# Kernel optimization log

Measured on AMD Instinct MI355X. Metric: run time of the kernel, lower is better.

The kernel has to match this reference:

```python
import jax, jax.numpy as jnp
import numpy as np

B, N, FIN, FOUT = 32, 1024, 128, 128
NEG_SLOPE = 0.01  # torch nn.LeakyReLU default


def setup_inputs() -> dict:
    key = jax.random.key(0)
    k1, k2, k3, k4 = jax.random.split(key, 4)
    node_mat = jax.random.normal(k1, (B, N, FIN), dtype=jnp.float32)
    adj_mat = jax.random.uniform(k2, (B, N, N), dtype=jnp.float32)
    # nn.Linear(FIN, FOUT): weight [FOUT, FIN], bias [FOUT]
    bound = 1.0 / np.sqrt(FIN)
    W = jax.random.uniform(k3, (FOUT, FIN), minval=-bound, maxval=bound, dtype=jnp.float32)
    b = jax.random.uniform(k4, (FOUT,), minval=-bound, maxval=bound, dtype=jnp.float32)
    return {"node_mat": node_mat, "adj_mat": adj_mat, "W": W, "b": b}


def reference(node_mat, adj_mat, W, b):
    # degree per node: row-sum of adjacency [B, N, 1]
    n_neighbors = adj_mat.sum(axis=-1, keepdims=True)
    # D^-1 A : the original builds eye*(1/deg) then bmm; algebraically a row scaling
    norm_adj = adj_mat / n_neighbors                      # [B, N, N]
    agg = jnp.einsum('bnm,bmf->bnf', norm_adj, node_mat)  # [B, N, FIN]
    out = jnp.einsum('bnf,of->bno', agg, W) + b           # [B, N, FOUT]
    return jnp.where(out >= 0, out, NEG_SLOPE * out)      # LeakyReLU
```

## Files before the change

### kernel.cpp

```cpp
#include <hip/hip_runtime.h>
#include <cstdint>
#include <cstddef>

#define BB   32
#define NN   1024
#define FIN  128
#define FOUT 128

typedef __attribute__((ext_vector_type(8))) short bf16x8;
typedef __attribute__((ext_vector_type(4))) float f32x4;

__device__ __forceinline__ unsigned int f2bf(float f) {
    union { float f; unsigned int u; } v; v.f = f;
    unsigned int u = v.u;
    return (u + 0x7FFFu + ((u >> 16) & 1u)) >> 16;
}
__device__ __forceinline__ unsigned int pack2(float a, float b) {
    return f2bf(a) | (f2bf(b) << 16);
}

__global__ __launch_bounds__(256) void y_kernel(const float* __restrict__ node,
                                                const float* __restrict__ W,
                                                unsigned short* __restrict__ Yt) {
    __shared__ unsigned short Wlds[128 * 136];
    __shared__ unsigned short Nlds[64 * 136];

    const int tid = threadIdx.x;
    const int bid = blockIdx.x;
    const int b   = bid >> 4;
    const int m0  = (bid & 15) * 64;

    #pragma unroll
    for (int i = 0; i < 16; ++i) {
        const int idx = i * 256 + tid;
        const int row = idx >> 5;
        const int c   = (idx & 31) * 4;
        float4 v = ((const float4*)W)[idx];
        uint2 p; p.x = pack2(v.x, v.y); p.y = pack2(v.z, v.w);
        *(uint2*)&Wlds[row * 136 + c] = p;
    }
    {
        const float* base = node + ((size_t)b * NN + m0) * FIN;
        #pragma unroll
        for (int i = 0; i < 8; ++i) {
            const int idx = i * 256 + tid;
            const int row = idx >> 5;
            const int c   = (idx & 31) * 4;
            float4 v = *(const float4*)(base + row * FIN + c);
            uint2 p; p.x = pack2(v.x, v.y); p.y = pack2(v.z, v.w);
            *(uint2*)&Nlds[row * 136 + c] = p;
        }
    }
    __syncthreads();

    const int w = tid >> 6, lane = tid & 63;
    const int wo = w * 32;
    const int lcol = lane & 15, lk = (lane >> 4) * 8;

    f32x4 acc[2][4] = {};
    #pragma unroll
    for (int kc = 0; kc < 4; ++kc) {
        const int kof = kc * 32 + lk;
        bf16x8 a[2], bb[4];
        #pragma unroll
        for (int mi = 0; mi < 2; ++mi)
            a[mi] = *(const bf16x8*)&Wlds[(wo + mi*16 + lcol) * 136 + kof];
        #pragma unroll
        for (int ni = 0; ni < 4; ++ni)
            bb[ni] = *(const bf16x8*)&Nlds[(ni*16 + lcol) * 136 + kof];
        #pragma unroll
        for (int mi = 0; mi < 2; ++mi)
            #pragma unroll
            for (int ni = 0; ni < 4; ++ni)
                acc[mi][ni] = __builtin_amdgcn_mfma_f32_16x16x32_bf16(
                    a[mi], bb[ni], acc[mi][ni], 0, 0, 0);
    }
    __syncthreads();

    unsigned short* Ylds = Wlds;
    const int rq = (lane >> 4) * 4;
    #pragma unroll
    for (int mi = 0; mi < 2; ++mi)
        #pragma unroll
        for (int ni = 0; ni < 4; ++ni)
            #pragma unroll
            for (int r = 0; r < 4; ++r) {
                const int o = wo + mi * 16 + rq + r;
                const int m = ni * 16 + lcol;
                Ylds[o * 72 + m] = (unsigned short)f2bf(acc[mi][ni][r]);
            }
    __syncthreads();

    {
        const int oq = tid >> 3, c = (tid & 7) * 8;
        #pragma unroll
        for (int j = 0; j < 4; ++j) {
            const int o = oq + 32 * j;
            uint4 v = *(const uint4*)&Ylds[o * 72 + c];
            *(uint4*)(Yt + ((size_t)b * FOUT + o) * NN + m0 + c) = v;
        }
    }
}

__global__ __launch_bounds__(256, 4) void gcn_kernel(const float* __restrict__ adj,
                                                     const unsigned short* __restrict__ Yt,
                                                     const float* __restrict__ bias,
                                                     float* __restrict__ out) {
    const int tid  = threadIdx.x;
    const int lane = tid & 63;
    const int w    = tid >> 6;

    const int raw = blockIdx.x;
    const int bid = (raw & 7) * 128 + (raw >> 3);
    const int b   = bid >> 5;
    const int n0  = (bid & 31) * 32;

    const int lcol = lane & 15, q = lane >> 4;
    const int wm = (w & 1) * 16;
    const int wn = (w >> 1) * 64;
    const int row  = n0 + wm + lcol;

    const float* aP = adj + ((size_t)b * NN + row) * NN + q * 8;
    const unsigned short* bP[4];
    #pragma unroll
    for (int ni = 0; ni < 4; ++ni)
        bP[ni] = Yt + ((size_t)b * FOUT + wn + ni * 16 + lcol) * NN + q * 8;

    f32x4 acc[4] = {};
    float rsum = 0.f;

    #pragma unroll 2
    for (int kc = 0; kc < 32; ++kc) {
        const float4 a0 = *(const float4*)(aP);
        const float4 a1 = *(const float4*)(aP + 4);
        aP += 32;
        rsum += ((a0.x + a0.y) + (a0.z + a0.w)) + ((a1.x + a1.y) + (a1.z + a1.w));
        uint4 pk;
        pk.x = pack2(a0.x, a0.y); pk.y = pack2(a0.z, a0.w);
        pk.z = pack2(a1.x, a1.y); pk.w = pack2(a1.z, a1.w);
        const bf16x8 a = *(const bf16x8*)&pk;
        #pragma unroll
        for (int ni = 0; ni < 4; ++ni) {
            const bf16x8 bb = *(const bf16x8*)bP[ni];
            bP[ni] += 32;
            acc[ni] = __builtin_amdgcn_mfma_f32_16x16x32_bf16(a, bb, acc[ni], 0, 0, 0);
        }
    }

    rsum += __shfl_xor(rsum, 16);
    rsum += __shfl_xor(rsum, 32);

    const int rq = q * 4;
    float sc[4];
    #pragma unroll
    for (int r = 0; r < 4; ++r) sc[r] = 1.0f / __shfl(rsum, rq + r);

    float* outB = out + ((size_t)(b * NN + n0 + wm)) * FOUT;
    #pragma unroll
    for (int ni = 0; ni < 4; ++ni) {
        const float bc = bias[wn + ni * 16 + lcol];
        #pragma unroll
        for (int r = 0; r < 4; ++r) {
            float v = acc[ni][r] * sc[r] + bc;
            v = (v >= 0.f) ? v : 0.01f * v;
            outB[(size_t)(rq + r) * FOUT + wn + ni * 16 + lcol] = v;
        }
    }
}

extern "C" void kernel_launch(void* const* d_in, const int* in_sizes, int n_in,
                              void* d_out, int out_size, void* d_ws, size_t ws_size,
                              hipStream_t stream) {
    const float* node = (const float*)d_in[0];
    const float* adj  = (const float*)d_in[1];
    const float* W    = (const float*)d_in[2];
    const float* bias = (const float*)d_in[3];
    float* out = (float*)d_out;
    unsigned short* Yt = (unsigned short*)d_ws;

    hipLaunchKernelGGL(y_kernel,   dim3(512),  dim3(256), 0, stream, node, W, Yt);
    hipLaunchKernelGGL(gcn_kernel, dim3(1024), dim3(256), 0, stream, adj, Yt, bias, out);
}
```

Before: 277.8 us.

## Stage adj and Yt tiles through double-buffered LDS with direct global-to-LDS loads

```diff
diff --git a/kernel.cpp b/kernel.cpp
--- a/kernel.cpp
+++ b/kernel.cpp
@@ -17,6 +17,12 @@
 }
 __device__ __forceinline__ unsigned int pack2(float a, float b) {
     return f2bf(a) | (f2bf(b) << 16);
+}
+
+__device__ __forceinline__ void load_lds16(const void* g, void* l) {
+    __builtin_amdgcn_global_load_lds(
+        (const __attribute__((address_space(1))) unsigned int*)g,
+        (__attribute__((address_space(3))) unsigned int*)l, 16, 0, 0);
 }
 
 __global__ __launch_bounds__(256) void y_kernel(const float* __restrict__ node,
@@ -102,10 +108,14 @@
     }
 }
 
+#define BUFB 12288
+
 __global__ __launch_bounds__(256, 4) void gcn_kernel(const float* __restrict__ adj,
                                                      const unsigned short* __restrict__ Yt,
                                                      const float* __restrict__ bias,
                                                      float* __restrict__ out) {
+    __shared__ char smem[2 * BUFB];
+
     const int tid  = threadIdx.x;
     const int lane = tid & 63;
     const int w    = tid >> 6;
@@ -118,34 +128,79 @@
     const int lcol = lane & 15, q = lane >> 4;
     const int wm = (w & 1) * 16;
     const int wn = (w >> 1) * 64;
-    const int row  = n0 + wm + lcol;
-
-    const float* aP = adj + ((size_t)b * NN + row) * NN + q * 8;
-    const unsigned short* bP[4];
-    #pragma unroll
-    for (int ni = 0; ni < 4; ++ni)
-        bP[ni] = Yt + ((size_t)b * FOUT + wn + ni * 16 + lcol) * NN + q * 8;
+
+    const int rA = w * 8 + (lane >> 3);
+    const int gA = (lane & 7) ^ (lane >> 3);
+    const float* aSrc = adj + ((size_t)(b * NN + n0 + rA)) * NN + gA * 4;
+    char* aDst = smem + w * 1024;
+
+    const unsigned short* bSrc[2];
+    char* bDst[2];
+    #pragma unroll
+    for (int j = 0; j < 2; ++j) {
+        const int s = (w * 2 + j) * 64 + lane;
+        const int o = s >> 2, c = s & 3;
+        const int g = c ^ (o & 3);
+        bSrc[j] = Yt + ((size_t)(b * FOUT + o)) * NN + g * 8;
+        bDst[j] = smem + 4096 + (w * 2 + j) * 1024;
+    }
+
+    const int R = wm + lcol, keyA = R & 7;
+    const int offA0 = (R * 8 + ((2 * q)     ^ keyA)) * 16;
+    const int offA1 = (R * 8 + ((2 * q + 1) ^ keyA)) * 16;
+    int offB[4];
+    #pragma unroll
+    for (int ni = 0; ni < 4; ++ni) {
+        const int o = wn + ni * 16 + lcol;
+        offB[ni] = 4096 + (o * 4 + (q ^ (o & 3))) * 16;
+    }
 
     f32x4 acc[4] = {};
     float rsum = 0.f;
 
-    #pragma unroll 2
-    for (int kc = 0; kc < 32; ++kc) {
-        const float4 a0 = *(const float4*)(aP);
-        const float4 a1 = *(const float4*)(aP + 4);
-        aP += 32;
-        rsum += ((a0.x + a0.y) + (a0.z + a0.w)) + ((a1.x + a1.y) + (a1.z + a1.w));
-        uint4 pk;
-        pk.x = pack2(a0.x, a0.y); pk.y = pack2(a0.z, a0.w);
-        pk.z = pack2(a1.x, a1.y); pk.w = pack2(a1.z, a1.w);
-        const bf16x8 a = *(const bf16x8*)&pk;
-        #pragma unroll
-        for (int ni = 0; ni < 4; ++ni) {
-            const bf16x8 bb = *(const bf16x8*)bP[ni];
-            bP[ni] += 32;
-            acc[ni] = __builtin_amdgcn_mfma_f32_16x16x32_bf16(a, bb, acc[ni], 0, 0, 0);
-        }
-    }
+    #define STAGE(buf, s)                                                  \
+        do {                                                               \
+            load_lds16(aSrc    + (s) * 32, aDst    + (buf) * BUFB);        \
+            load_lds16(bSrc[0] + (s) * 32, bDst[0] + (buf) * BUFB);        \
+            load_lds16(bSrc[1] + (s) * 32, bDst[1] + (buf) * BUFB);        \
+        } while (0)
+
+    #define COMPUTE(buf)                                                   \
+        do {                                                               \
+            const char* base = smem + (buf) * BUFB;                        \
+            const float4 f0 = *(const float4*)(base + offA0);              \
+            const float4 f1 = *(const float4*)(base + offA1);              \
+            rsum += ((f0.x + f0.y) + (f0.z + f0.w))                        \
+                  + ((f1.x + f1.y) + (f1.z + f1.w));                       \
+            uint4 pk;                                                      \
+            pk.x = pack2(f0.x, f0.y); pk.y = pack2(f0.z, f0.w);            \
+            pk.z = pack2(f1.x, f1.y); pk.w = pack2(f1.z, f1.w);            \
+            const bf16x8 a = *(const bf16x8*)&pk;                          \
+            _Pragma("unroll")                                              \
+            for (int ni = 0; ni < 4; ++ni) {                               \
+                const bf16x8 bbf = *(const bf16x8*)(base + offB[ni]);      \
+                acc[ni] = __builtin_amdgcn_mfma_f32_16x16x32_bf16(         \
+                    a, bbf, acc[ni], 0, 0, 0);                             \
+            }                                                              \
+        } while (0)
+
+    STAGE(0, 0);
+    asm volatile("s_waitcnt vmcnt(0)" ::: "memory");
+    __builtin_amdgcn_s_barrier();
+
+    for (int t = 0; t < 16; ++t) {
+        STAGE(1, 2 * t + 1);
+        COMPUTE(0);
+        asm volatile("s_waitcnt vmcnt(0)" ::: "memory");
+        __builtin_amdgcn_s_barrier();
+
+        if (t < 15) STAGE(0, 2 * t + 2);
+        COMPUTE(1);
+        asm volatile("s_waitcnt vmcnt(0)" ::: "memory");
+        __builtin_amdgcn_s_barrier();
+    }
+    #undef STAGE
+    #undef COMPUTE
 
     rsum += __shfl_xor(rsum, 16);
     rsum += __shfl_xor(rsum, 32);
```

After: 234.9 us. -15.4%, faster.

## Stage adjacency through LDS with coalesced loads and pre-swizzle Y fragments

Applied to the files above, without the earlier changes.

```diff
diff --git a/kernel.cpp b/kernel.cpp
--- a/kernel.cpp
+++ b/kernel.cpp
@@ -92,12 +92,18 @@
     __syncthreads();
 
     {
-        const int oq = tid >> 3, c = (tid & 7) * 8;
+        const int lcol2 = tid & 15, q2 = (tid >> 4) & 3, p = tid >> 6;
+        const int kc0 = m0 >> 5;
         #pragma unroll
         for (int j = 0; j < 4; ++j) {
-            const int o = oq + 32 * j;
-            uint4 v = *(const uint4*)&Ylds[o * 72 + c];
-            *(uint4*)(Yt + ((size_t)b * FOUT + o) * NN + m0 + c) = v;
+            const int pr  = p + j * 4;
+            const int kcl = pr >> 3;
+            const int ni  = pr & 7;
+            const int o    = ni * 16 + lcol2;
+            const int mloc = kcl * 32 + q2 * 8;
+            uint4 v = *(const uint4*)&Ylds[o * 72 + mloc];
+            *(uint4*)(Yt + (((size_t)((b * 32 + kc0 + kcl) * 8 + ni)) * 64
+                            + (tid & 63)) * 8) = v;
         }
     }
 }
@@ -106,6 +112,8 @@
                                                      const unsigned short* __restrict__ Yt,
                                                      const float* __restrict__ bias,
                                                      float* __restrict__ out) {
+    __shared__ float Alds[4][2][16 * 68];
+
     const int tid  = threadIdx.x;
     const int lane = tid & 63;
     const int w    = tid >> 6;
@@ -118,34 +126,79 @@
     const int lcol = lane & 15, q = lane >> 4;
     const int wm = (w & 1) * 16;
     const int wn = (w >> 1) * 64;
-    const int row  = n0 + wm + lcol;
-
-    const float* aP = adj + ((size_t)b * NN + row) * NN + q * 8;
-    const unsigned short* bP[4];
-    #pragma unroll
-    for (int ni = 0; ni < 4; ++ni)
-        bP[ni] = Yt + ((size_t)b * FOUT + wn + ni * 16 + lcol) * NN + q * 8;
+
+    const int arow = lane >> 2;
+    const int ac4  = (lane & 3) * 4;
+    const float* aSrc = adj + ((size_t)(b * NN + n0 + wm + arow)) * NN + ac4;
+    float* aBuf0 = &Alds[w][0][arow * 68 + ac4];
+    float* aBuf1 = &Alds[w][1][arow * 68 + ac4];
+    const float* aRd0 = &Alds[w][0][lcol * 68];
+    const float* aRd1 = &Alds[w][1][lcol * 68];
+
+    const unsigned short* bPtr =
+        Yt + ((size_t)(b * 32) * 8 + (wn >> 4)) * 512 + (size_t)lane * 8;
 
     f32x4 acc[4] = {};
     float rsum = 0.f;
 
+    float4 av[4];
+    uint4  bfr[2][4];
+
+    #define GLOADA(t_)                                                        \
+        do { _Pragma("unroll")                                                \
+            for (int i = 0; i < 4; ++i)                                       \
+                av[i] = *(const float4*)(aSrc + (t_) * 64 + i * 16);          \
+        } while (0)
+    #define DSWRA(bufp)                                                       \
+        do { _Pragma("unroll")                                                \
+            for (int i = 0; i < 4; ++i)                                       \
+                *(float4*)((bufp) + i * 16) = av[i];                          \
+        } while (0)
+    #define GLOADB(slot, kc_)                                                 \
+        do { _Pragma("unroll")                                                \
+            for (int ni = 0; ni < 4; ++ni)                                    \
+                bfr[slot][ni] = *(const uint4*)(bPtr +                        \
+                    ((size_t)((kc_) * 8 + ni)) * 512);                        \
+        } while (0)
+    #define KCSTEP(rdp, kcl, slot)                                            \
+        do {                                                                  \
+            const float4 f0 = *(const float4*)((rdp) + (kcl) * 32 + q * 8);   \
+            const float4 f1 = *(const float4*)((rdp) + (kcl) * 32 + q * 8 + 4);\
+            rsum += ((f0.x + f0.y) + (f0.z + f0.w))                           \
+                  + ((f1.x + f1.y) + (f1.z + f1.w));                          \
+            uint4 pk;                                                         \
+            pk.x = pack2(f0.x, f0.y); pk.y = pack2(f0.z, f0.w);               \
+            pk.z = pack2(f1.x, f1.y); pk.w = pack2(f1.z, f1.w);               \
+            const bf16x8 a = *(const bf16x8*)&pk;                             \
+            _Pragma("unroll")                                                 \
+            for (int ni = 0; ni < 4; ++ni) {                                  \
+                const bf16x8 bbf = *(const bf16x8*)&bfr[slot][ni];            \
+                acc[ni] = __builtin_amdgcn_mfma_f32_16x16x32_bf16(            \
+                    a, bbf, acc[ni], 0, 0, 0);                                \
+            }                                                                 \
+        } while (0)
+
+    GLOADA(0);
+    DSWRA(aBuf0);
+    GLOADA(1);
+    GLOADB(0, 0);
+    GLOADB(1, 1);
+
     #pragma unroll 2
-    for (int kc = 0; kc < 32; ++kc) {
-        const float4 a0 = *(const float4*)(aP);
-        const float4 a1 = *(const float4*)(aP + 4);
-        aP += 32;
-        rsum += ((a0.x + a0.y) + (a0.z + a0.w)) + ((a1.x + a1.y) + (a1.z + a1.w));
-        uint4 pk;
-        pk.x = pack2(a0.x, a0.y); pk.y = pack2(a0.z, a0.w);
-        pk.z = pack2(a1.x, a1.y); pk.w = pack2(a1.z, a1.w);
-        const bf16x8 a = *(const bf16x8*)&pk;
-        #pragma unroll
-        for (int ni = 0; ni < 4; ++ni) {
-            const bf16x8 bb = *(const bf16x8*)bP[ni];
-            bP[ni] += 32;
-            acc[ni] = __builtin_amdgcn_mfma_f32_16x16x32_bf16(a, bb, acc[ni], 0, 0, 0);
-        }
-    }
+    for (int t = 0; t < 16; ++t) {
+        float*       wrBuf = (t & 1) ? aBuf0 : aBuf1;
+        const float* rdBuf = (t & 1) ? aRd1  : aRd0;
+        if (t < 15) DSWRA(wrBuf);
+        if (t < 14) GLOADA(t + 2);
+        KCSTEP(rdBuf, 0, 0);
+        if (t < 15) GLOADB(0, 2 * t + 2);
+        KCSTEP(rdBuf, 1, 1);
+        if (t < 15) GLOADB(1, 2 * t + 3);
+    }
+    #undef GLOADA
+    #undef DSWRA
+    #undef GLOADB
+    #undef KCSTEP
 
     rsum += __shfl_xor(rsum, 16);
     rsum += __shfl_xor(rsum, 32);
```

Result: slower. 299.0 us (+7.6%).

## Stage adjacency and Yt tiles in LDS via async loads with multi-buffer pipeline

Applied to the files above, without the earlier changes.

```diff
diff --git a/kernel.cpp b/kernel.cpp
--- a/kernel.cpp
+++ b/kernel.cpp
@@ -17,6 +17,12 @@
 }
 __device__ __forceinline__ unsigned int pack2(float a, float b) {
     return f2bf(a) | (f2bf(b) << 16);
+}
+
+__device__ __forceinline__ void load_lds16(const void* g, void* l) {
+    __builtin_amdgcn_global_load_lds(
+        (const __attribute__((address_space(1))) unsigned int*)g,
+        (__attribute__((address_space(3))) unsigned int*)l, 16, 0, 0);
 }
 
 __global__ __launch_bounds__(256) void y_kernel(const float* __restrict__ node,
@@ -102,50 +108,118 @@
     }
 }
 
-__global__ __launch_bounds__(256, 4) void gcn_kernel(const float* __restrict__ adj,
-                                                     const unsigned short* __restrict__ Yt,
-                                                     const float* __restrict__ bias,
-                                                     float* __restrict__ out) {
+#define ABYTES 16384
+#define BBYTES 8192
+#define BUFB   (ABYTES + BBYTES)
+
+__global__ __launch_bounds__(1024, 4) void gcn_kernel(const float* __restrict__ adj,
+                                                      const unsigned short* __restrict__ Yt,
+                                                      const float* __restrict__ bias,
+                                                      float* __restrict__ out) {
+    __shared__ __align__(16) char smem[4 * BUFB];
+
     const int tid  = threadIdx.x;
     const int lane = tid & 63;
     const int w    = tid >> 6;
 
     const int raw = blockIdx.x;
-    const int bid = (raw & 7) * 128 + (raw >> 3);
-    const int b   = bid >> 5;
-    const int n0  = (bid & 31) * 32;
+    const int bid = (raw & 7) * 32 + (raw >> 3);
+    const int b   = bid >> 3;
+    const int n0  = (bid & 7) * 128;
 
     const int lcol = lane & 15, q = lane >> 4;
-    const int wm = (w & 1) * 16;
-    const int wn = (w >> 1) * 64;
-    const int row  = n0 + wm + lcol;
-
-    const float* aP = adj + ((size_t)b * NN + row) * NN + q * 8;
-    const unsigned short* bP[4];
-    #pragma unroll
-    for (int ni = 0; ni < 4; ++ni)
-        bP[ni] = Yt + ((size_t)b * FOUT + wn + ni * 16 + lcol) * NN + q * 8;
+    const int wm = (w & 7) * 16;
+    const int wn = (w >> 3) * 64;
+
+    const char* src0 = nullptr; const char* src1 = nullptr;
+    char* dst0 = nullptr; char* dst1 = nullptr;
+    int sstride = 0;
+    if (w < 8) {
+        const int i0 = 2 * w, i1 = 2 * w + 1;
+        const int r0 = i0 * 8 + (lane >> 3), r1 = i1 * 8 + (lane >> 3);
+        const int g0 = (lane & 7) ^ (r0 & 7), g1 = (lane & 7) ^ (r1 & 7);
+        src0 = (const char*)(adj + ((size_t)(b * NN + n0 + r0)) * NN + g0 * 4);
+        src1 = (const char*)(adj + ((size_t)(b * NN + n0 + r1)) * NN + g1 * 4);
+        dst0 = smem + i0 * 1024;
+        dst1 = smem + i1 * 1024;
+        sstride = 128;
+    } else if (w < 12) {
+        const int j0 = 2 * (w - 8), j1 = j0 + 1;
+        const int o0 = j0 * 16 + (lane >> 2), o1 = j1 * 16 + (lane >> 2);
+        const int g0 = (lane & 3) ^ (o0 & 3), g1 = (lane & 3) ^ (o1 & 3);
+        src0 = (const char*)(Yt + ((size_t)(b * FOUT + o0)) * NN + g0 * 8);
+        src1 = (const char*)(Yt + ((size_t)(b * FOUT + o1)) * NN + g1 * 8);
+        dst0 = smem + ABYTES + j0 * 1024;
+        dst1 = smem + ABYTES + j1 * 1024;
+        sstride = 64;
+    }
+
+    const int R = wm + lcol, keyR = R & 7;
+    const int offA0 = R * 128 + ((2 * q)     ^ keyR) * 16;
+    const int offA1 = R * 128 + ((2 * q + 1) ^ keyR) * 16;
+    int offB[4];
+    #pragma unroll
+    for (int ni = 0; ni < 4; ++ni) {
+        const int o = wn + ni * 16 + lcol;
+        offB[ni] = ABYTES + o * 64 + (q ^ (o & 3)) * 16;
+    }
 
     f32x4 acc[4] = {};
     float rsum = 0.f;
 
-    #pragma unroll 2
-    for (int kc = 0; kc < 32; ++kc) {
-        const float4 a0 = *(const float4*)(aP);
-        const float4 a1 = *(const float4*)(aP + 4);
-        aP += 32;
-        rsum += ((a0.x + a0.y) + (a0.z + a0.w)) + ((a1.x + a1.y) + (a1.z + a1.w));
-        uint4 pk;
-        pk.x = pack2(a0.x, a0.y); pk.y = pack2(a0.z, a0.w);
-        pk.z = pack2(a1.x, a1.y); pk.w = pack2(a1.z, a1.w);
-        const bf16x8 a = *(const bf16x8*)&pk;
-        #pragma unroll
-        for (int ni = 0; ni < 4; ++ni) {
-            const bf16x8 bb = *(const bf16x8*)bP[ni];
-            bP[ni] += 32;
-            acc[ni] = __builtin_amdgcn_mfma_f32_16x16x32_bf16(a, bb, acc[ni], 0, 0, 0);
-        }
-    }
+    #define STAGE(buf, s)                                                   \
+        do {                                                                \
+            if (w < 12) {                                                   \
+                load_lds16(src0 + (s) * sstride, dst0 + (buf) * BUFB);      \
+                load_lds16(src1 + (s) * sstride, dst1 + (buf) * BUFB);      \
+            }                                                               \
+        } while (0)
+
+    #define COMPUTE(buf)                                                    \
+        do {                                                                \
+            const char* base = smem + (buf) * BUFB;                         \
+            const float4 f0 = *(const float4*)(base + offA0);               \
+            const float4 f1 = *(const float4*)(base + offA1);               \
+            rsum += ((f0.x + f0.y) + (f0.z + f0.w))                         \
+                  + ((f1.x + f1.y) + (f1.z + f1.w));                        \
+            uint4 pk;                                                       \
+            pk.x = pack2(f0.x, f0.y); pk.y = pack2(f0.z, f0.w);             \
+            pk.z = pack2(f1.x, f1.y); pk.w = pack2(f1.z, f1.w);             \
+            const bf16x8 a = *(const bf16x8*)&pk;                           \
+            _Pragma("unroll")                                               \
+            for (int ni = 0; ni < 4; ++ni) {                                \
+                const bf16x8 bbf = *(const bf16x8*)(base + offB[ni]);       \
+                acc[ni] = __builtin_amdgcn_mfma_f32_16x16x32_bf16(          \
+                    a, bbf, acc[ni], 0, 0, 0);                              \
+            }                                                               \
+        } while (0)
+
+    STAGE(0, 0);
+    STAGE(1, 1);
+
+    #pragma unroll 4
+    for (int t = 0; t < 28; ++t) {
+        STAGE((t + 2) & 3, t + 2);
+        asm volatile("s_waitcnt vmcnt(4)" ::: "memory");
+        __builtin_amdgcn_s_barrier();
+        COMPUTE(t & 3);
+    }
+    STAGE(2, 30);
+    asm volatile("s_waitcnt vmcnt(4)" ::: "memory");
+    __builtin_amdgcn_s_barrier();
+    COMPUTE(0);
+    STAGE(3, 31);
+    asm volatile("s_waitcnt vmcnt(4)" ::: "memory");
+    __builtin_amdgcn_s_barrier();
+    COMPUTE(1);
+    asm volatile("s_waitcnt vmcnt(2)" ::: "memory");
+    __builtin_amdgcn_s_barrier();
+    COMPUTE(2);
+    asm volatile("s_waitcnt vmcnt(0)" ::: "memory");
+    __builtin_amdgcn_s_barrier();
+    COMPUTE(3);
+    #undef STAGE
+    #undef COMPUTE
 
     rsum += __shfl_xor(rsum, 16);
     rsum += __shfl_xor(rsum, 32);
@@ -178,6 +252,6 @@
     float* out = (float*)d_out;
     unsigned short* Yt = (unsigned short*)d_ws;
 
-    hipLaunchKernelGGL(y_kernel,   dim3(512),  dim3(256), 0, stream, node, W, Yt);
-    hipLaunchKernelGGL(gcn_kernel, dim3(1024), dim3(256), 0, stream, adj, Yt, bias, out);
-}
+    hipLaunchKernelGGL(y_kernel,   dim3(512), dim3(256),  0, stream, node, W, Yt);
+    hipLaunchKernelGGL(gcn_kernel, dim3(256), dim3(1024), 0, stream, adj, Yt, bias, out);
+}
```

After: 229.4 us. 1.21x faster.
